# Kernel optimization log

Hardware: AMD Instinct MI355X
Metric: run time of the kernel (lower is better)

## Reference

```python
import jax, jax.numpy as jnp
import numpy as np

N_HEAD = 12
D_MODEL = 768
B, T = 1, 1024


def _rope(x):
    # x: (B, H, T, Dh). Matches torch RoPE: split even/odd, cat halves.
    Dh = x.shape[-1]
    t = x.shape[2]
    inv_freq = 1.0 / (10000.0 ** (jnp.arange(0, Dh, 2, dtype=jnp.float32) / Dh))
    freqs = jnp.arange(t, dtype=jnp.float32)[:, None] * inv_freq[None, :]  # (T, Dh/2)
    cos = jnp.cos(freqs)[None, None]  # (1,1,T,Dh/2)
    sin = jnp.sin(freqs)[None, None]
    x1 = x[..., 0::2]
    x2 = x[..., 1::2]
    return jnp.concatenate([-x2 * sin + x1 * cos, x1 * sin + x2 * cos], axis=-1)


def _wedge(x, A, id_bias):
    # S = (A - A^T) + diag(id_bias_h), per head h; x: (B,H,T,Dh)
    skew = A - A.T  # (Dh, Dh)
    S = skew[None, :, :] + jax.vmap(jnp.diag)(id_bias)  # (H, Dh, Dh)
    flow = jnp.einsum('bhtd,hde->bhte', x, S)
    return x + flow


def _forward(x, WV_w, WV_b, WK_w, WK_b, WQ_w, A, id_bias, sink, v_nulls, WO_w, WO_b):
    b, t, c = x.shape
    n_br = WO_w.shape[0]
    n_sh = n_br
    dh = c // n_br
    h_tot = n_br * n_sh
    scale = dh ** -0.5

    q = (x @ WQ_w).reshape(b, t, h_tot, dh).transpose(0, 2, 1, 3)      # (B,Htot,T,Dh)
    k_base = (x @ WK_w + WK_b).reshape(b, t, n_sh, dh).transpose(0, 2, 1, 3)
    v_base = (x @ WV_w + WV_b).reshape(b, t, n_sh, dh).transpose(0, 2, 1, 3)
    k = jnp.tile(k_base, (1, n_br, 1, 1))  # (B,Htot,T,Dh)
    v = jnp.tile(v_base, (1, n_br, 1, 1))

    q = _rope(_wedge(q, A, id_bias))
    k = _rope(_wedge(k, A, id_bias))

    scores = jnp.einsum('bhtd,bhsd->bhts', q, k) * scale  # (B,Htot,T,T)
    causal = jnp.tril(jnp.ones((t, t), dtype=bool))
    scores = jnp.where(causal[None, None], scores, -jnp.inf)

    sinks = jnp.broadcast_to(sink.reshape(1, h_tot, 1, 1), (b, h_tot, t, 1))
    probs = jax.nn.softmax(jnp.concatenate([scores, sinks], axis=-1), axis=-1)
    probs_tok, probs_sink = probs[..., :t], probs[..., t:]

    out_tok = jnp.einsum('bhts,bhsd->bhtd', probs_tok, v)
    out_sink = probs_sink * v_nulls.reshape(h_tot, dh)[None, :, None, :]
    ctx = out_tok + out_sink  # (B,Htot,T,Dh)

    ctx = ctx.reshape(b, n_br, n_sh, t, dh).transpose(0, 1, 3, 2, 4).reshape(b, n_br, t, c)
    y = jnp.einsum('bntc,ncd->bntd', ctx, WO_w) + WO_b[None, :, None, :]
    return y.mean(axis=1)  # (B,T,C)


def setup_inputs() -> dict:
    key = jax.random.key(0)
    ks = jax.random.split(key, 12)
    c = D_MODEL
    n_br = N_HEAD
    dh = c // n_br
    h_tot = n_br * n_br
    s = 0.02
    return {
        'x': jax.random.normal(ks[0], (B, T, c), dtype=jnp.float32),
        'WV_w': jax.random.normal(ks[1], (c, c), dtype=jnp.float32) * s,
        'WV_b': jnp.zeros((c,), dtype=jnp.float32),
        'WK_w': jax.random.normal(ks[2], (c, c), dtype=jnp.float32) * s,
        'WK_b': jnp.zeros((c,), dtype=jnp.float32),
        'WQ_w': jax.random.normal(ks[3], (c, c * n_br), dtype=jnp.float32) * s,
        'A': jax.random.normal(ks[4], (dh, dh), dtype=jnp.float32) * s,
        'id_bias': jax.random.normal(ks[5], (h_tot, dh), dtype=jnp.float32) * s,
        'sink': jax.random.normal(ks[6], (h_tot,), dtype=jnp.float32) * s,
        'v_nulls': jax.random.normal(ks[7], (n_br, c), dtype=jnp.float32) * s,
        'WO_w': jax.random.normal(ks[8], (n_br, c, c), dtype=jnp.float32) * (1.0 / np.sqrt(c)),
        'WO_b': jnp.zeros((n_br, c), dtype=jnp.float32),
    }


def reference(x, WV_w, WV_b, WK_w, WK_b, WQ_w, A, id_bias, sink, v_nulls, WO_w, WO_b):
    return _forward(x, WV_w, WV_b, WK_w, WK_b, WQ_w, A, id_bias, sink, v_nulls, WO_w, WO_b)
```

## Files before the change

kernel.cpp:

```cpp
#include <hip/hip_runtime.h>
#include <hip/hip_bf16.h>

#define T_SEQ   1024
#define C_MODEL 768
#define N_BR    12
#define DH      64
#define H_TOT   144
#define NQ      9216

typedef __bf16 bf16x8 __attribute__((ext_vector_type(8)));
typedef float  f32x4  __attribute__((ext_vector_type(4)));
typedef unsigned int u32x4 __attribute__((ext_vector_type(4)));
typedef unsigned short u16;

#define SM_OFF 3.0f
#define LOG2E  1.44269504089f
#define QSCALE (0.125f * LOG2E)

__device__ __forceinline__ void gload16(void* lds, const void* g)
{
    __builtin_amdgcn_global_load_lds(
        (const __attribute__((address_space(1))) void*)g,
        (__attribute__((address_space(3))) void*)lds, 16, 0, 0);
}

__device__ __forceinline__ void split1(float x, u16& h, u16& l)
{
    __bf16 bh = (__bf16)x;
    __bf16 bl = (__bf16)(x - (float)bh);
    h = __builtin_bit_cast(u16, bh);
    l = __builtin_bit_cast(u16, bl);
}

__device__ __forceinline__ u16 tobf(float x)
{
    return __builtin_bit_cast(u16, (__bf16)x);
}

__device__ __forceinline__ unsigned cvtpk(float a, float b)
{
    unsigned r;
    asm("v_cvt_pk_bf16_f32 %0, %1, %2" : "=v"(r) : "v"(a), "v"(b));
    return r;
}

__device__ __forceinline__ float exp2raw(float x)
{
    float r;
    asm("v_exp_f32 %0, %1" : "=v"(r) : "v"(x));
    return r;
}

__device__ __forceinline__ int xcd_swz(int bid, int nwg)
{
    return (bid & 7) * (nwg >> 3) + (bid >> 3);
}

__device__ __forceinline__ int swb(int row, int byteoff)
{
    return row * 128 + (byteoff ^ ((row & 7) << 4));
}

__device__ __forceinline__ bf16x8 ldsr8(const u16* p, int byteoff)
{
    return *reinterpret_cast<const bf16x8*>(reinterpret_cast<const char*>(p) + byteoff);
}

__device__ __forceinline__ void convt_body(const float* __restrict__ W,
                                           u16* __restrict__ out, int K, int N,
                                           int nx, int ky, float (*t)[33], int tid)
{
    const int n0 = nx * 32;
    const int k0 = ky * 32;
    const int tx = tid & 31;
    const int ty = tid >> 5;
    #pragma unroll
    for (int r = 0; r < 4; ++r)
        t[ty + r * 8][tx] = W[(size_t)(k0 + ty + r * 8) * N + n0 + tx];
    __syncthreads();
    #pragma unroll
    for (int r = 0; r < 4; ++r)
        out[(size_t)(n0 + ty + r * 8) * K + k0 + tx] = tobf(t[tx][ty + r * 8]);
}

__global__ __launch_bounds__(256)
void prep_kernel(const float* __restrict__ x, u16* __restrict__ xh,
                 const float* __restrict__ Amat, const float* __restrict__ id_bias,
                 u16* __restrict__ Mth, u16* __restrict__ Mtl,
                 const float* __restrict__ WO_b, float* __restrict__ mbias,
                 float* __restrict__ tab,
                 const float* __restrict__ WO_w, u16* __restrict__ wot,
                 const float* __restrict__ WK_w, const float* __restrict__ WV_w,
                 u16* __restrict__ wkvt)
{
    __shared__ float tsh[32][33];
    const int b   = blockIdx.x;
    const int tid = threadIdx.x;

    if (b < 128) {
        const int idx = b * 256 + tid;
        const int t = idx >> 5, i = idx & 31;
        const float inv = expf(-(float)i * (logf(10000.f) / 32.f));
        const float fr = (float)t * inv;
        tab[t * 64 + i]      = cosf(fr);
        tab[t * 64 + 32 + i] = sinf(fr);
    } else if (b < 272) {
        const int h = b - 128;
        const int base = tid * 16;
        #pragma unroll
        for (int i = 0; i < 16; ++i) {
            const int idx = base + i;
            const int e = idx >> 6, d = idx & 63;
            float v = Amat[d * 64 + e] - Amat[e * 64 + d];
            if (d == e) v += 1.0f + id_bias[h * 64 + d];
            u16 hh, ll;
            split1(v, hh, ll);
            Mth[(size_t)h * 4096 + idx] = hh;
            Mtl[(size_t)h * 4096 + idx] = ll;
        }
    } else if (b < 275) {
        const int d = (b - 272) * 256 + tid;
        if (d < C_MODEL) {
            float s = 0.f;
            #pragma unroll
            for (int n = 0; n < N_BR; ++n) s += WO_b[n * C_MODEL + d];
            mbias[d] = s * (1.0f / 12.0f);
        }
    } else if (b < 1043) {
        const size_t i = (size_t)(b - 275) * 1024 + tid * 4;
        float4 v = *reinterpret_cast<const float4*>(&x[i]);
        ushort4 o = { tobf(v.x), tobf(v.y), tobf(v.z), tobf(v.w) };
        *reinterpret_cast<ushort4*>(&xh[i]) = o;
    } else if (b < 7955) {
        const int u = b - 1043;
        convt_body(WO_w, wot, NQ, C_MODEL, u % 24, u / 24, tsh, tid);
    } else if (b < 8531) {
        const int u = b - 7955;
        convt_body(WK_w, wkvt, C_MODEL, C_MODEL, u % 24, u / 24, tsh, tid);
    } else {
        const int u = b - 8531;
        convt_body(WV_w, wkvt + 589824, C_MODEL, C_MODEL, u % 24, u / 24, tsh, tid);
    }
}

#define BM 128
#define BN 128
#define BK 32

__global__ __launch_bounds__(256)
void gemm_bf16_kernel(const u16* __restrict__ A, const u16* __restrict__ B,
                      float* __restrict__ Cp, int M, int N, int K,
                      int nx, int ny, int nz)
{
    __shared__ __align__(16) u16 sA[2][BM * BK], sB[2][BN * BK];

    const int nwg = nx * ny * nz;
    const int wg  = xcd_swz(blockIdx.x, nwg);
    const int x   = wg % nx;
    const int y   = (wg / nx) % ny;
    const int z   = wg / (nx * ny);

    const int tid  = threadIdx.x;
    const int lane = tid & 63;
    const int wid  = tid >> 6;
    const int m0   = y * BM;
    const int n0   = x * BN;
    const int kc   = K / nz;
    const int kbeg = z * kc;
    const int kend = kbeg + kc;

    const int wm = (wid >> 1) * 64;
    const int wn = (wid & 1) * 64;

    f32x4 acc[4][4];
    #pragma unroll
    for (int i = 0; i < 4; ++i)
        #pragma unroll
        for (int j = 0; j < 4; ++j)
            #pragma unroll
            for (int r = 0; r < 4; ++r) acc[i][j][r] = 0.f;

    const int r0 = tid >> 2;
    const int c0 = tid & 3;
    const int rA = wm + (lane & 15);
    const int rB = wn + (lane & 15);
    const int co = (lane >> 4) * 8;

    auto STAGE = [&](int buf, int k0) {
        gload16(&sA[buf][(size_t)tid * 8],         &A[(size_t)(m0 + r0)      * K + k0 + c0 * 8]);
        gload16(&sA[buf][(size_t)(tid + 256) * 8], &A[(size_t)(m0 + r0 + 64) * K + k0 + c0 * 8]);
        gload16(&sB[buf][(size_t)tid * 8],         &B[(size_t)(n0 + r0)      * K + k0 + c0 * 8]);
        gload16(&sB[buf][(size_t)(tid + 256) * 8], &B[(size_t)(n0 + r0 + 64) * K + k0 + c0 * 8]);
    };

    STAGE(0, kbeg);
    __syncthreads();
    int cur = 0;
    for (int k0 = kbeg; k0 < kend; k0 += BK) {
        if (k0 + BK < kend) STAGE(cur ^ 1, k0 + BK);

        bf16x8 ah[4], bh[4];
        #pragma unroll
        for (int i = 0; i < 4; ++i)
            ah[i] = *reinterpret_cast<const bf16x8*>(&sA[cur][(size_t)(rA + i * 16) * BK + co]);
        #pragma unroll
        for (int j = 0; j < 4; ++j)
            bh[j] = *reinterpret_cast<const bf16x8*>(&sB[cur][(size_t)(rB + j * 16) * BK + co]);
        #pragma unroll
        for (int i = 0; i < 4; ++i)
            #pragma unroll
            for (int j = 0; j < 4; ++j)
                acc[i][j] = __builtin_amdgcn_mfma_f32_16x16x32_bf16(ah[i], bh[j], acc[i][j], 0, 0, 0);
        __syncthreads();
        cur ^= 1;
    }

    float* Cz = Cp + (size_t)z * M * N;
    const int crow0 = m0 + wm + (lane >> 4) * 4;
    const int ccol0 = n0 + wn + (lane & 15);
    #pragma unroll
    for (int i = 0; i < 4; ++i)
        #pragma unroll
        for (int j = 0; j < 4; ++j)
            #pragma unroll
            for (int r = 0; r < 4; ++r)
                Cz[(size_t)(crow0 + i * 16 + r) * N + ccol0 + j * 16] = acc[i][j][r];
}

__global__ __launch_bounds__(256)
void gemm64_kernel(const u16* __restrict__ A, const u16* __restrict__ B,
                   float* __restrict__ Cp, int M, int N, int K,
                   int nx, int ny, int nz)
{
    __shared__ __align__(16) u16 sA[2][64 * BK], sB[2][128 * BK];

    const int nwg = nx * ny * nz;
    const int wg  = xcd_swz(blockIdx.x, nwg);
    const int x   = wg % nx;
    const int y   = (wg / nx) % ny;
    const int z   = wg / (nx * ny);

    const int tid  = threadIdx.x;
    const int lane = tid & 63;
    const int wid  = tid >> 6;
    const int m0   = y * 64;
    const int n0   = x * 128;
    const int kc   = K / nz;
    const int kbeg = z * kc;
    const int kend = kbeg + kc;

    const int wm = (wid >> 1) * 32;
    const int wn = (wid & 1) * 64;
    const int g  = lane >> 4;
    const int li = lane & 15;

    f32x4 acc[2][4];
    #pragma unroll
    for (int i = 0; i < 2; ++i)
        #pragma unroll
        for (int j = 0; j < 4; ++j)
            #pragma unroll
            for (int r = 0; r < 4; ++r) acc[i][j][r] = 0.f;

    const int r0 = tid >> 2;
    const int c0 = (tid & 3) * 8;

    auto STAGE = [&](int buf, int k0) {
        gload16(&sA[buf][(size_t)tid * 8],         &A[(size_t)(m0 + r0)      * K + k0 + c0]);
        gload16(&sB[buf][(size_t)tid * 8],         &B[(size_t)(n0 + r0)      * K + k0 + c0]);
        gload16(&sB[buf][(size_t)(tid + 256) * 8], &B[(size_t)(n0 + r0 + 64) * K + k0 + c0]);
    };

    STAGE(0, kbeg);
    __syncthreads();
    int cur = 0;
    for (int k0 = kbeg; k0 < kend; k0 += BK) {
        if (k0 + BK < kend) STAGE(cur ^ 1, k0 + BK);

        bf16x8 ah[2], bh[4];
        #pragma unroll
        for (int i = 0; i < 2; ++i)
            ah[i] = *reinterpret_cast<const bf16x8*>(&sA[cur][(size_t)(wm + 16 * i + li) * BK + g * 8]);
        #pragma unroll
        for (int j = 0; j < 4; ++j)
            bh[j] = *reinterpret_cast<const bf16x8*>(&sB[cur][(size_t)(wn + 16 * j + li) * BK + g * 8]);
        #pragma unroll
        for (int i = 0; i < 2; ++i)
            #pragma unroll
            for (int j = 0; j < 4; ++j)
                acc[i][j] = __builtin_amdgcn_mfma_f32_16x16x32_bf16(ah[i], bh[j], acc[i][j], 0, 0, 0);
        __syncthreads();
        cur ^= 1;
    }

    float* Cz = Cp + (size_t)z * M * N;
    const int crow0 = m0 + wm + g * 4;
    const int ccol0 = n0 + wn + li;
    #pragma unroll
    for (int i = 0; i < 2; ++i)
        #pragma unroll
        for (int j = 0; j < 4; ++j)
            #pragma unroll
            for (int r = 0; r < 4; ++r)
                Cz[(size_t)(crow0 + i * 16 + r) * N + ccol0 + j * 16] = acc[i][j][r];
}

__global__ __launch_bounds__(256)
void gemm_q_rope_kernel(const u16* __restrict__ A, const u16* __restrict__ B,
                        const float* __restrict__ tab, u16* __restrict__ Q2)
{
    __shared__ __align__(16) u16 sA[2][64 * BK], sB[2][128 * BK];

    const int K = C_MODEL;
    const int wg = xcd_swz(blockIdx.x, 1152);
    const int y  = wg & 15;
    const int x  = wg >> 4;

    const int tid  = threadIdx.x;
    const int lane = tid & 63;
    const int wid  = tid >> 6;
    const int m0   = y * 64;
    const int n0   = x * 128;

    const int wm = (wid >> 1) * 32;
    const int wn = (wid & 1) * 64;
    const int g  = lane >> 4;
    const int li = lane & 15;

    f32x4 acc[2][4];
    #pragma unroll
    for (int i = 0; i < 2; ++i)
        #pragma unroll
        for (int j = 0; j < 4; ++j)
            #pragma unroll
            for (int r = 0; r < 4; ++r) acc[i][j][r] = 0.f;

    const int r0 = tid >> 2;
    const int c0 = (tid & 3) * 8;

    auto STAGE = [&](int buf, int k0) {
        gload16(&sA[buf][(size_t)tid * 8],         &A[(size_t)(m0 + r0)      * K + k0 + c0]);
        gload16(&sB[buf][(size_t)tid * 8],         &B[(size_t)(n0 + r0)      * K + k0 + c0]);
        gload16(&sB[buf][(size_t)(tid + 256) * 8], &B[(size_t)(n0 + r0 + 64) * K + k0 + c0]);
    };

    STAGE(0, 0);
    __syncthreads();
    int cur = 0;
    for (int k0 = 0; k0 < K; k0 += BK) {
        if (k0 + BK < K) STAGE(cur ^ 1, k0 + BK);

        bf16x8 ah[2], bh[4];
        #pragma unroll
        for (int i = 0; i < 2; ++i)
            ah[i] = *reinterpret_cast<const bf16x8*>(&sA[cur][(size_t)(wm + 16 * i + li) * BK + g * 8]);
        #pragma unroll
        for (int j = 0; j < 4; ++j)
            bh[j] = *reinterpret_cast<const bf16x8*>(&sB[cur][(size_t)(wn + 16 * j + li) * BK + g * 8]);
        #pragma unroll
        for (int i = 0; i < 2; ++i)
            #pragma unroll
            for (int j = 0; j < 4; ++j)
                acc[i][j] = __builtin_amdgcn_mfma_f32_16x16x32_bf16(ah[i], bh[j], acc[i][j], 0, 0, 0);
        __syncthreads();
        cur ^= 1;
    }

    const int h  = (n0 + wn) >> 6;
    const bool ev = (li & 1) == 0;
    #pragma unroll
    for (int j = 0; j < 4; ++j) {
        const int e  = j * 16 + li;
        const int i2 = e >> 1;
        #pragma unroll
        for (int i = 0; i < 2; ++i) {
            #pragma unroll
            for (int r = 0; r < 4; ++r) {
                const int t = m0 + wm + i * 16 + g * 4 + r;
                const float own = acc[i][j][r];
                const float oth = __shfl_xor(own, 1);
                const float cs = tab[t * 64 + i2];
                const float sn = tab[t * 64 + 32 + i2];
                float o; int ch;
                if (ev) { o = own * cs - oth * sn; ch = i2; }
                else    { o = oth * sn + own * cs; ch = 32 + i2; }
                Q2[((size_t)h * T_SEQ + t) * 64 + ch] = tobf(o * QSCALE);
            }
        }
    }
}

__global__ __launch_bounds__(256)
void reduce_kernel(const float* __restrict__ part, float* __restrict__ out,
                   const float* __restrict__ bias, int MN, int N, int Z, float alpha)
{
    const int i = (blockIdx.x * 256 + threadIdx.x) * 4;
    if (i >= MN) return;
    float4 s = *reinterpret_cast<const float4*>(&part[i]);
    for (int z = 1; z < Z; ++z) {
        float4 p = *reinterpret_cast<const float4*>(&part[(size_t)z * MN + i]);
        s.x += p.x; s.y += p.y; s.z += p.z; s.w += p.w;
    }
    s.x *= alpha; s.y *= alpha; s.z *= alpha; s.w *= alpha;
    if (bias) {
        const int c = i % N;
        s.x += bias[c]; s.y += bias[c + 1]; s.z += bias[c + 2]; s.w += bias[c + 3];
    }
    *reinterpret_cast<float4*>(&out[i]) = s;
}

__global__ __launch_bounds__(256)
void reduce_kv_kernel(const float* __restrict__ part, float* __restrict__ out,
                      const float* __restrict__ kb, const float* __restrict__ vb,
                      int MN, int Z)
{
    const int i = (blockIdx.x * 256 + threadIdx.x) * 4;
    if (i >= MN) return;
    float4 s = *reinterpret_cast<const float4*>(&part[i]);
    for (int z = 1; z < Z; ++z) {
        float4 p = *reinterpret_cast<const float4*>(&part[(size_t)z * MN + i]);
        s.x += p.x; s.y += p.y; s.z += p.z; s.w += p.w;
    }
    const int c = i % 1536;
    const float* bp = (c < 768) ? (kb + c) : (vb + c - 768);
    s.x += bp[0]; s.y += bp[1]; s.z += bp[2]; s.w += bp[3];
    *reinterpret_cast<float4*>(&out[i]) = s;
}

__global__ __launch_bounds__(256)
void fold_wq_kernel(const float* __restrict__ WQ, const u16* __restrict__ Mth,
                    const u16* __restrict__ Mtl, u16* __restrict__ wqt)
{
    __shared__ __align__(16) u16 sMh[4096], sMl[4096];
    __shared__ __align__(16) u16 sB[8192];

    const int h   = blockIdx.x;
    const int k0  = blockIdx.y * 128;
    const int tid = threadIdx.x;
    const int lane = tid & 63, w = tid >> 6, g = lane >> 4, li = lane & 15;

    {
        const char* gmh = (const char*)(Mth + (size_t)h * 4096);
        const char* gml = (const char*)(Mtl + (size_t)h * 4096);
        #pragma unroll
        for (int p = 0; p < 2; ++p) {
            const int u = p * 256 + tid;
            const int row = u >> 3, off = (u & 7) * 16;
            const int src = swb(row, off);
            gload16((char*)sMh + u * 16, gmh + src);
            gload16((char*)sMl + u * 16, gml + src);
        }
    }
    {
        const int r    = tid >> 1;
        const int half = tid & 1;
        const float* src = WQ + (size_t)(k0 + r) * NQ + h * 64 + half * 32;
        #pragma unroll
        for (int q = 0; q < 8; ++q) {
            float4 v = *reinterpret_cast<const float4*>(&src[q * 4]);
            ushort4 o = { tobf(v.x), tobf(v.y), tobf(v.z), tobf(v.w) };
            const int byte = swb(r, half * 64 + q * 8);
            *reinterpret_cast<ushort4*>(reinterpret_cast<char*>(sB) + byte) = o;
        }
    }
    __syncthreads();

    f32x4 acc[4][2];
    #pragma unroll
    for (int i = 0; i < 4; ++i)
        #pragma unroll
        for (int jj = 0; jj < 2; ++jj)
            #pragma unroll
            for (int r = 0; r < 4; ++r) acc[i][jj][r] = 0.f;

    bf16x8 ah[4][2], al[4][2];
    #pragma unroll
    for (int i = 0; i < 4; ++i)
        #pragma unroll
        for (int ks = 0; ks < 2; ++ks) {
            ah[i][ks] = ldsr8(sMh, swb(16 * i + li, ks * 64 + g * 16));
            al[i][ks] = ldsr8(sMl, swb(16 * i + li, ks * 64 + g * 16));
        }
    #pragma unroll
    for (int jj = 0; jj < 2; ++jj) {
        const int brow = 16 * (2 * w + jj) + li;
        #pragma unroll
        for (int ks = 0; ks < 2; ++ks) {
            bf16x8 bh = ldsr8(sB, swb(brow, ks * 64 + g * 16));
            #pragma unroll
            for (int i = 0; i < 4; ++i) {
                acc[i][jj] = __builtin_amdgcn_mfma_f32_16x16x32_bf16(ah[i][ks], bh, acc[i][jj], 0, 0, 0);
                acc[i][jj] = __builtin_amdgcn_mfma_f32_16x16x32_bf16(al[i][ks], bh, acc[i][jj], 0, 0, 0);
            }
        }
    }

    #pragma unroll
    for (int i = 0; i < 4; ++i)
        #pragma unroll
        for (int jj = 0; jj < 2; ++jj) {
            const int kc = k0 + 16 * (2 * w + jj) + li;
            #pragma unroll
            for (int r = 0; r < 4; ++r) {
                const int e = 16 * i + g * 4 + r;
                wqt[((size_t)h * 64 + e) * 768 + kc] = tobf(acc[i][jj][r]);
            }
        }
}

__global__ __launch_bounds__(256)
void wedge_vt_kernel(const float* __restrict__ KV, u16* __restrict__ K2,
                     u16* __restrict__ Vt,
                     const u16* __restrict__ Mth, const u16* __restrict__ Mtl,
                     const float* __restrict__ tab)
{
    __shared__ __align__(16) char smem[24576];
    const int b   = blockIdx.x;
    const int t0  = blockIdx.y * 64;
    const int tid = threadIdx.x;

    if (b < H_TOT) {
        u16* sX  = (u16*)smem;
        u16* sMh = (u16*)(smem + 8192);
        u16* sMl = (u16*)(smem + 16384);
        const int h = b;
        const int lane = tid & 63, w = tid >> 6, g = lane >> 4, li = lane & 15;

        {
            const int r  = tid >> 2;
            const int c0 = (tid & 3) * 16;
            const float* xrow = KV + (size_t)(t0 + r) * 1536 + (h % N_BR) * 64;
            #pragma unroll
            for (int q = 0; q < 4; ++q) {
                const int c = c0 + q * 4;
                float4 v = *reinterpret_cast<const float4*>(&xrow[c]);
                ushort4 hv = { tobf(v.x), tobf(v.y), tobf(v.z), tobf(v.w) };
                *reinterpret_cast<ushort4*>((char*)sX + swb(r, 2 * c)) = hv;
            }
        }
        {
            const char* gmh = (const char*)(Mth + (size_t)h * 4096);
            const char* gml = (const char*)(Mtl + (size_t)h * 4096);
            #pragma unroll
            for (int u = 0; u < 2; ++u) {
                const int L = (u * 256 + tid) * 16;
                const int row = L >> 7, off = L & 127;
                const int src = swb(row, off);
                gload16((char*)sMh + L, gmh + src);
                gload16((char*)sMl + L, gml + src);
            }
        }
        __syncthreads();

        f32x4 acc[4];
        #pragma unroll
        for (int j = 0; j < 4; ++j)
            #pragma unroll
            for (int r = 0; r < 4; ++r) acc[j][r] = 0.f;

        bf16x8 ah[2];
        #pragma unroll
        for (int ks = 0; ks < 2; ++ks)
            ah[ks] = ldsr8(sX, swb(w * 16 + li, ks * 64 + g * 16));
        #pragma unroll
        for (int ks = 0; ks < 2; ++ks)
            #pragma unroll
            for (int j = 0; j < 4; ++j) {
                bf16x8 bh = ldsr8(sMh, swb(16 * j + li, ks * 64 + g * 16));
                bf16x8 bl = ldsr8(sMl, swb(16 * j + li, ks * 64 + g * 16));
                acc[j] = __builtin_amdgcn_mfma_f32_16x16x32_bf16(ah[ks], bh, acc[j], 0, 0, 0);
                acc[j] = __builtin_amdgcn_mfma_f32_16x16x32_bf16(ah[ks], bl, acc[j], 0, 0, 0);
            }

        const bool ev = (li & 1) == 0;
        #pragma unroll
        for (int j = 0; j < 4; ++j) {
            const int e = 16 * j + li;
            const int i2 = e >> 1;
            #pragma unroll
            for (int r = 0; r < 4; ++r) {
                const int t = t0 + w * 16 + g * 4 + r;
                const float own = acc[j][r];
                const float oth = __shfl_xor(own, 1);
                const float cs = tab[t * 64 + i2];
                const float sn = tab[t * 64 + 32 + i2];
                float o; int ch;
                if (ev) { o = own * cs - oth * sn; ch = i2; }
                else    { o = oth * sn + own * cs; ch = 32 + i2; }
                K2[((size_t)h * T_SEQ + t) * 64 + ch] = tobf(o);
            }
        }
    } else {
        float (*Ls)[65] = (float (*)[65])smem;
        const int s = b - H_TOT;
        {
            const int r  = tid >> 2;
            const int c0 = (tid & 3) * 16;
            const float* row = KV + (size_t)(t0 + r) * 1536 + 768 + s * 64;
            #pragma unroll
            for (int q = 0; q < 4; ++q) {
                float4 v = *reinterpret_cast<const float4*>(&row[c0 + q * 4]);
                Ls[r][c0 + q * 4 + 0] = v.x; Ls[r][c0 + q * 4 + 1] = v.y;
                Ls[r][c0 + q * 4 + 2] = v.z; Ls[r][c0 + q * 4 + 3] = v.w;
            }
        }
        __syncthreads();
        {
            const int d  = tid >> 2;
            const int tq = (tid & 3) * 16;
            u16* orow = Vt + ((size_t)s * 64 + d) * T_SEQ + t0 + tq;
            #pragma unroll
            for (int q = 0; q < 4; ++q) {
                ushort4 o;
                o.x = tobf(Ls[tq + q * 4 + 0][d]);
                o.y = tobf(Ls[tq + q * 4 + 1][d]);
                o.z = tobf(Ls[tq + q * 4 + 2][d]);
                o.w = tobf(Ls[tq + q * 4 + 3][d]);
                *reinterpret_cast<ushort4*>(&orow[q * 4]) = o;
            }
        }
    }
}

__device__ __forceinline__ void attn_stage_kv(
    int buf, int kv0, int h, int s, int tid,
    const u16* __restrict__ K2, const u16* __restrict__ Vt,
    u16* sK, u16* sV)
{
    const char* gk = (const char*)(K2 + ((size_t)h * T_SEQ + kv0) * 64);
    const char* gv = (const char*)Vt + (size_t)s * 131072 + kv0 * 2;
    #pragma unroll
    for (int p = 0; p < 2; ++p) {
        const int u = p * 256 + tid;
        const int row = u >> 3;
        const int off = (u & 7) * 16;
        const int sw  = off ^ ((row & 7) << 4);
        const int j  = row >> 4, g2 = (row >> 2) & 3, rr = row & 3;
        const int srow = 32 * (j & 1) + 8 * g2 + 4 * (j >> 1) + rr;
        gload16((char*)sK + buf * 8192 + u * 16, gk + srow * 128 + sw);
        gload16((char*)sV + buf * 8192 + u * 16, gv + row * 2048 + sw);
    }
}

template<bool DIAG>
__device__ __forceinline__ void attn_tile_sw(
    int kv0, int qglob, int g, int li,
    const u16* sK, const u16* sV, const bf16x8* qa, const bf16x8 ones,
    f32x4* acc, f32x4& psacc)
{
    f32x4 sacc[4];
    #pragma unroll
    for (int j = 0; j < 4; ++j)
        #pragma unroll
        for (int r = 0; r < 4; ++r) sacc[j][r] = -SM_OFF * LOG2E;

    __builtin_amdgcn_s_setprio(1);
    #pragma unroll
    for (int ks = 0; ks < 2; ++ks)
        #pragma unroll
        for (int j = 0; j < 4; ++j) {
            bf16x8 kb = ldsr8(sK, swb(16 * j + li, ks * 64 + g * 16));
            sacc[j] = __builtin_amdgcn_mfma_f32_16x16x32_bf16(kb, qa[ks], sacc[j], 0, 0, 0);
        }
    __builtin_amdgcn_s_setprio(0);

    float p[4][4];
    const int kvb = kv0 + 8 * g;
    #pragma unroll
    for (int j = 0; j < 4; ++j)
        #pragma unroll
        for (int r = 0; r < 4; ++r) {
            float sv_ = sacc[j][r];
            if (DIAG) {
                const int kv = kvb + 32 * (j & 1) + 4 * (j >> 1) + r;
                if (kv > qglob) sv_ = -__builtin_inff();
            }
            p[j][r] = exp2raw(sv_);
        }

    __builtin_amdgcn_s_setprio(1);
    #pragma unroll
    for (int ks = 0; ks < 2; ++ks) {
        u32x4 pw;
        pw[0] = cvtpk(p[ks][0],     p[ks][1]);
        pw[1] = cvtpk(p[ks][2],     p[ks][3]);
        pw[2] = cvtpk(p[ks + 2][0], p[ks + 2][1]);
        pw[3] = cvtpk(p[ks + 2][2], p[ks + 2][3]);
        bf16x8 pa = __builtin_bit_cast(bf16x8, pw);
        psacc = __builtin_amdgcn_mfma_f32_16x16x32_bf16(ones, pa, psacc, 0, 0, 0);
        #pragma unroll
        for (int j = 0; j < 4; ++j) {
            bf16x8 vb = ldsr8(sV, swb(16 * j + li, ks * 64 + g * 16));
            acc[j] = __builtin_amdgcn_mfma_f32_16x16x32_bf16(vb, pa, acc[j], 0, 0, 0);
        }
    }
    __builtin_amdgcn_s_setprio(0);
}

__global__ __launch_bounds__(256)
void attn_mfma_kernel(const u16* __restrict__ Q2, const u16* __restrict__ K2,
                      const u16* __restrict__ Vt, const float* __restrict__ sink,
                      const float* __restrict__ v_nulls, u16* __restrict__ ctxb)
{
    const int h  = blockIdx.x;
    const int qt = 15 - (int)blockIdx.y;
    const int s  = h % N_BR;
    const int tid  = threadIdx.x;
    const int lane = tid & 63, w = tid >> 6, g = lane >> 4, li = lane & 15;

    __shared__ __align__(16) u16 sK[8192];
    __shared__ __align__(16) u16 sV[8192];

    const u16* qrow = Q2 + ((size_t)h * T_SEQ + qt * 64 + w * 16 + li) * 64;
    bf16x8 qa[2];
    qa[0] = *reinterpret_cast<const bf16x8*>(qrow + g * 8);
    qa[1] = *reinterpret_cast<const bf16x8*>(qrow + 32 + g * 8);

    bf16x8 ones;
    #pragma unroll
    for (int e = 0; e < 8; ++e) ones[e] = (__bf16)1.0f;

    attn_stage_kv(0, 0, h, s, tid, K2, Vt, sK, sV);

    f32x4 acc[4];
    #pragma unroll
    for (int j = 0; j < 4; ++j)
        #pragma unroll
        for (int r = 0; r < 4; ++r) acc[j][r] = 0.f;
    f32x4 psacc;
    #pragma unroll
    for (int r = 0; r < 4; ++r) psacc[r] = 0.f;

    __syncthreads();

    const int qglob = qt * 64 + w * 16 + li;
    const int nt = qt + 1;
    int cur = 0;
    for (int kt = 0; kt < nt - 1; ++kt) {
        attn_stage_kv(cur ^ 1, (kt + 1) * 64, h, s, tid, K2, Vt, sK, sV);
        attn_tile_sw<false>(kt * 64, qglob, g, li,
                            sK + cur * 4096, sV + cur * 4096, qa, ones, acc, psacc);
        __syncthreads();
        cur ^= 1;
    }
    attn_tile_sw<true>(qt * 64, qglob, g, li,
                       sK + cur * 4096, sV + cur * 4096, qa, ones, acc, psacc);

    const float es = __expf(sink[h] - SM_OFF);
    const float rz = 1.0f / (psacc[0] + es);

    const int t = qt * 64 + w * 16 + li;
    u16* orow = ctxb + (size_t)t * NQ + h * 64;
    const float* vn = v_nulls + h * 64;
    #pragma unroll
    for (int j = 0; j < 4; ++j) {
        const int d0 = 16 * j + 4 * g;
        float4 vnv = *reinterpret_cast<const float4*>(&vn[d0]);
        ushort4 o;
        o.x = tobf((acc[j][0] + es * vnv.x) * rz);
        o.y = tobf((acc[j][1] + es * vnv.y) * rz);
        o.z = tobf((acc[j][2] + es * vnv.z) * rz);
        o.w = tobf((acc[j][3] + es * vnv.w) * rz);
        *reinterpret_cast<ushort4*>(&orow[d0]) = o;
    }
}

extern "C" void kernel_launch(void* const* d_in, const int* in_sizes, int n_in,
                              void* d_out, int out_size, void* d_ws, size_t ws_size,
                              hipStream_t stream)
{
    (void)in_sizes; (void)n_in; (void)out_size; (void)ws_size;

    const float* x       = (const float*)d_in[0];
    const float* WV_w    = (const float*)d_in[1];
    const float* WV_b    = (const float*)d_in[2];
    const float* WK_w    = (const float*)d_in[3];
    const float* WK_b    = (const float*)d_in[4];
    const float* WQ_w    = (const float*)d_in[5];
    const float* Amat    = (const float*)d_in[6];
    const float* id_bias = (const float*)d_in[7];
    const float* sink    = (const float*)d_in[8];
    const float* v_nulls = (const float*)d_in[9];
    const float* WO_w    = (const float*)d_in[10];
    const float* WO_b    = (const float*)d_in[11];
    float* out = (float*)d_out;

    float* tab    = (float*)d_ws;
    float* mbias  = tab + 65536;
    float* kvbase = mbias + 768;
    u16* Mth  = (u16*)(kvbase + 1572864);
    u16* Mtl  = Mth + 589824;
    u16* xh   = Mtl + 589824;
    u16* wqt  = xh + 786432;
    u16* wkvt = wqt + 7077888;
    u16* wot  = wkvt + 1179648;
    u16* K2   = wot + 7077888;
    u16* Vt   = K2 + 9437184;
    u16* Q2   = Vt + 786432;
    u16* ctxb = Q2 + 9437184;
    float* pkv = (float*)(ctxb + 9437184);

    float* outpart = (float*)K2;

    const dim3 blk(256);

    prep_kernel<<<dim3(9107), blk, 0, stream>>>(
        x, xh, Amat, id_bias, Mth, Mtl, WO_b, mbias, tab, WO_w, wot, WK_w, WV_w, wkvt);

    fold_wq_kernel<<<dim3(H_TOT, 6), blk, 0, stream>>>(WQ_w, Mth, Mtl, wqt);

    gemm_bf16_kernel<<<dim3(384), blk, 0, stream>>>(
        xh, wkvt, pkv, T_SEQ, 1536, C_MODEL, 12, 8, 4);
    reduce_kv_kernel<<<dim3(1536), blk, 0, stream>>>(pkv, kvbase, WK_b, WV_b, 1572864, 4);

    wedge_vt_kernel<<<dim3(156, 16), blk, 0, stream>>>(
        kvbase, K2, Vt, Mth, Mtl, tab);

    gemm_q_rope_kernel<<<dim3(1152), blk, 0, stream>>>(xh, wqt, tab, Q2);

    attn_mfma_kernel<<<dim3(H_TOT, 16), blk, 0, stream>>>(
        Q2, K2, Vt, sink, v_nulls, ctxb);

    gemm64_kernel<<<dim3(768), blk, 0, stream>>>(
        ctxb, wot, outpart, T_SEQ, C_MODEL, NQ, 6, 16, 8);
    reduce_kernel<<<dim3(768), blk, 0, stream>>>(
        outpart, out, mbias, 786432, C_MODEL, 8, 1.0f / 12.0f);
}
```

Baseline: 167.3 us.

## Triple-buffer GEMM LDS pipelines with vmcnt waits and enlarge Q-GEMM tiles

Replaces the double-buffered LDS staging in the three GEMM kernels with a three-stage ring. Each iteration waits on vmcnt for the oldest stage and issues one barrier, replacing the two __syncthreads per iteration, so global loads stay in flight two tiles ahead. The Q-projection GEMM also moves from 64x128 to 128x128 tiles, halving the grid to 576 workgroups and reusing each A/B fragment across more MFMAs. This costs more LDS and accumulator registers, which may lower occupancy. Dropping the trailing barrier leaves the three-buffer rotation as the only protection against write-after-read hazards.

```diff
diff --git a/kernel.cpp b/kernel.cpp
--- a/kernel.cpp
+++ b/kernel.cpp
@@ -50,6 +50,11 @@
     asm("v_exp_f32 %0, %1" : "=v"(r) : "v"(x));
     return r;
 }
+
+#define PIPE_WAIT(N_STR)                                        \
+    asm volatile("s_waitcnt vmcnt(" N_STR ")" ::: "memory");    \
+    __builtin_amdgcn_s_barrier();                               \
+    __builtin_amdgcn_sched_barrier(0);
 
 __device__ __forceinline__ int xcd_swz(int bid, int nwg)
 {
@@ -152,7 +157,7 @@
                       float* __restrict__ Cp, int M, int N, int K,
                       int nx, int ny, int nz)
 {
-    __shared__ __align__(16) u16 sA[2][BM * BK], sB[2][BN * BK];
+    __shared__ __align__(16) u16 sA[3][BM * BK], sB[3][BN * BK];
 
     const int nwg = nx * ny * nz;
     const int wg  = xcd_swz(blockIdx.x, nwg);
@@ -194,25 +199,27 @@
     };
 
     STAGE(0, kbeg);
-    __syncthreads();
-    int cur = 0;
-    for (int k0 = kbeg; k0 < kend; k0 += BK) {
-        if (k0 + BK < kend) STAGE(cur ^ 1, k0 + BK);
-
+    STAGE(1, kbeg + BK);
+    int kt = 0;
+    for (int k0 = kbeg; k0 < kend; k0 += BK, ++kt) {
+        if (k0 + BK >= kend) { PIPE_WAIT("0"); }
+        else                 { PIPE_WAIT("4"); }
+        if (k0 + 2 * BK < kend) STAGE((kt + 2) % 3, k0 + 2 * BK);
+
+        const u16* cA = sA[kt % 3];
+        const u16* cB = sB[kt % 3];
         bf16x8 ah[4], bh[4];
         #pragma unroll
         for (int i = 0; i < 4; ++i)
-            ah[i] = *reinterpret_cast<const bf16x8*>(&sA[cur][(size_t)(rA + i * 16) * BK + co]);
+            ah[i] = *reinterpret_cast<const bf16x8*>(&cA[(size_t)(rA + i * 16) * BK + co]);
         #pragma unroll
         for (int j = 0; j < 4; ++j)
-            bh[j] = *reinterpret_cast<const bf16x8*>(&sB[cur][(size_t)(rB + j * 16) * BK + co]);
+            bh[j] = *reinterpret_cast<const bf16x8*>(&cB[(size_t)(rB + j * 16) * BK + co]);
         #pragma unroll
         for (int i = 0; i < 4; ++i)
             #pragma unroll
             for (int j = 0; j < 4; ++j)
                 acc[i][j] = __builtin_amdgcn_mfma_f32_16x16x32_bf16(ah[i], bh[j], acc[i][j], 0, 0, 0);
-        __syncthreads();
-        cur ^= 1;
     }
 
     float* Cz = Cp + (size_t)z * M * N;
@@ -232,7 +239,7 @@
                    float* __restrict__ Cp, int M, int N, int K,
                    int nx, int ny, int nz)
 {
-    __shared__ __align__(16) u16 sA[2][64 * BK], sB[2][128 * BK];
+    __shared__ __align__(16) u16 sA[3][64 * BK], sB[3][128 * BK];
 
     const int nwg = nx * ny * nz;
     const int wg  = xcd_swz(blockIdx.x, nwg);
@@ -272,25 +279,27 @@
     };
 
     STAGE(0, kbeg);
-    __syncthreads();
-    int cur = 0;
-    for (int k0 = kbeg; k0 < kend; k0 += BK) {
-        if (k0 + BK < kend) STAGE(cur ^ 1, k0 + BK);
-
+    STAGE(1, kbeg + BK);
+    int kt = 0;
+    for (int k0 = kbeg; k0 < kend; k0 += BK, ++kt) {
+        if (k0 + BK >= kend) { PIPE_WAIT("0"); }
+        else                 { PIPE_WAIT("3"); }
+        if (k0 + 2 * BK < kend) STAGE((kt + 2) % 3, k0 + 2 * BK);
+
+        const u16* cA = sA[kt % 3];
+        const u16* cB = sB[kt % 3];
         bf16x8 ah[2], bh[4];
         #pragma unroll
         for (int i = 0; i < 2; ++i)
-            ah[i] = *reinterpret_cast<const bf16x8*>(&sA[cur][(size_t)(wm + 16 * i + li) * BK + g * 8]);
+            ah[i] = *reinterpret_cast<const bf16x8*>(&cA[(size_t)(wm + 16 * i + li) * BK + g * 8]);
         #pragma unroll
         for (int j = 0; j < 4; ++j)
-            bh[j] = *reinterpret_cast<const bf16x8*>(&sB[cur][(size_t)(wn + 16 * j + li) * BK + g * 8]);
+            bh[j] = *reinterpret_cast<const bf16x8*>(&cB[(size_t)(wn + 16 * j + li) * BK + g * 8]);
         #pragma unroll
         for (int i = 0; i < 2; ++i)
             #pragma unroll
             for (int j = 0; j < 4; ++j)
                 acc[i][j] = __builtin_amdgcn_mfma_f32_16x16x32_bf16(ah[i], bh[j], acc[i][j], 0, 0, 0);
-        __syncthreads();
-        cur ^= 1;
     }
 
     float* Cz = Cp + (size_t)z * M * N;
@@ -309,61 +318,67 @@
 void gemm_q_rope_kernel(const u16* __restrict__ A, const u16* __restrict__ B,
                         const float* __restrict__ tab, u16* __restrict__ Q2)
 {
-    __shared__ __align__(16) u16 sA[2][64 * BK], sB[2][128 * BK];
+    __shared__ __align__(16) u16 sA[3][BM * BK], sB[3][BN * BK];
 
     const int K = C_MODEL;
-    const int wg = xcd_swz(blockIdx.x, 1152);
-    const int y  = wg & 15;
-    const int x  = wg >> 4;
+    const int wg = xcd_swz(blockIdx.x, 576);
+    const int y  = wg & 7;
+    const int x  = wg >> 3;
 
     const int tid  = threadIdx.x;
     const int lane = tid & 63;
     const int wid  = tid >> 6;
-    const int m0   = y * 64;
-    const int n0   = x * 128;
-
-    const int wm = (wid >> 1) * 32;
+    const int m0   = y * BM;
+    const int n0   = x * BN;
+
+    const int wm = (wid >> 1) * 64;
     const int wn = (wid & 1) * 64;
     const int g  = lane >> 4;
     const int li = lane & 15;
 
-    f32x4 acc[2][4];
-    #pragma unroll
-    for (int i = 0; i < 2; ++i)
+    f32x4 acc[4][4];
+    #pragma unroll
+    for (int i = 0; i < 4; ++i)
         #pragma unroll
         for (int j = 0; j < 4; ++j)
             #pragma unroll
             for (int r = 0; r < 4; ++r) acc[i][j][r] = 0.f;
 
     const int r0 = tid >> 2;
-    const int c0 = (tid & 3) * 8;
+    const int c0 = tid & 3;
+    const int rA = wm + li;
+    const int rB = wn + li;
+    const int co = g * 8;
 
     auto STAGE = [&](int buf, int k0) {
-        gload16(&sA[buf][(size_t)tid * 8],         &A[(size_t)(m0 + r0)      * K + k0 + c0]);
-        gload16(&sB[buf][(size_t)tid * 8],         &B[(size_t)(n0 + r0)      * K + k0 + c0]);
-        gload16(&sB[buf][(size_t)(tid + 256) * 8], &B[(size_t)(n0 + r0 + 64) * K + k0 + c0]);
+        gload16(&sA[buf][(size_t)tid * 8],         &A[(size_t)(m0 + r0)      * K + k0 + c0 * 8]);
+        gload16(&sA[buf][(size_t)(tid + 256) * 8], &A[(size_t)(m0 + r0 + 64) * K + k0 + c0 * 8]);
+        gload16(&sB[buf][(size_t)tid * 8],         &B[(size_t)(n0 + r0)      * K + k0 + c0 * 8]);
+        gload16(&sB[buf][(size_t)(tid + 256) * 8], &B[(size_t)(n0 + r0 + 64) * K + k0 + c0 * 8]);
     };
 
     STAGE(0, 0);
-    __syncthreads();
-    int cur = 0;
-    for (int k0 = 0; k0 < K; k0 += BK) {
-        if (k0 + BK < K) STAGE(cur ^ 1, k0 + BK);
-
-        bf16x8 ah[2], bh[4];
-        #pragma unroll
-        for (int i = 0; i < 2; ++i)
-            ah[i] = *reinterpret_cast<const bf16x8*>(&sA[cur][(size_t)(wm + 16 * i + li) * BK + g * 8]);
+    STAGE(1, BK);
+    int kt = 0;
+    for (int k0 = 0; k0 < K; k0 += BK, ++kt) {
+        if (k0 + BK >= K) { PIPE_WAIT("0"); }
+        else              { PIPE_WAIT("4"); }
+        if (k0 + 2 * BK < K) STAGE((kt + 2) % 3, k0 + 2 * BK);
+
+        const u16* cA = sA[kt % 3];
+        const u16* cB = sB[kt % 3];
+        bf16x8 ah[4], bh[4];
+        #pragma unroll
+        for (int i = 0; i < 4; ++i)
+            ah[i] = *reinterpret_cast<const bf16x8*>(&cA[(size_t)(rA + i * 16) * BK + co]);
         #pragma unroll
         for (int j = 0; j < 4; ++j)
-            bh[j] = *reinterpret_cast<const bf16x8*>(&sB[cur][(size_t)(wn + 16 * j + li) * BK + g * 8]);
-        #pragma unroll
-        for (int i = 0; i < 2; ++i)
+            bh[j] = *reinterpret_cast<const bf16x8*>(&cB[(size_t)(rB + j * 16) * BK + co]);
+        #pragma unroll
+        for (int i = 0; i < 4; ++i)
             #pragma unroll
             for (int j = 0; j < 4; ++j)
                 acc[i][j] = __builtin_amdgcn_mfma_f32_16x16x32_bf16(ah[i], bh[j], acc[i][j], 0, 0, 0);
-        __syncthreads();
-        cur ^= 1;
     }
 
     const int h  = (n0 + wn) >> 6;
@@ -373,7 +388,7 @@
         const int e  = j * 16 + li;
         const int i2 = e >> 1;
         #pragma unroll
-        for (int i = 0; i < 2; ++i) {
+        for (int i = 0; i < 4; ++i) {
             #pragma unroll
             for (int r = 0; r < 4; ++r) {
                 const int t = m0 + wm + i * 16 + g * 4 + r;
@@ -816,7 +831,7 @@
     wedge_vt_kernel<<<dim3(156, 16), blk, 0, stream>>>(
         kvbase, K2, Vt, Mth, Mtl, tab);
 
-    gemm_q_rope_kernel<<<dim3(1152), blk, 0, stream>>>(xh, wqt, tab, Q2);
+    gemm_q_rope_kernel<<<dim3(576), blk, 0, stream>>>(xh, wqt, tab, Q2);
 
     attn_mfma_kernel<<<dim3(H_TOT, 16), blk, 0, stream>>>(
         Q2, K2, Vt, sink, v_nulls, ctxb);
```

Result: slower. 185.3 us (+10.7%).
